# Optimization experiments

Measured on AMD Instinct MI355X. Metric: run time of the kernel, lower is better.

## Reference

```python
import jax, jax.numpy as jnp
from jax import lax
import numpy as np

N_X, N_Y, N_OBS = 30, 50, 256
ITERS, LR = 400, 0.05


def project_simplex(v):
    # Euclidean projection of a 1-D vector onto the probability simplex.
    n = v.shape[0]
    u = jnp.sort(v)[::-1]
    css = jnp.cumsum(u) - 1.0
    idx = jnp.arange(1, n + 1, dtype=v.dtype)
    rho = jnp.sum((u - css / idx) > 0)
    tau = jnp.take(css, rho - 1) / rho.astype(v.dtype)
    return jnp.maximum(v - tau, 0.0)


def worst_case(r, delta):
    # Exact value of the Ben-Tal et al. total-variation DRO inner problem:
    #   min_{eta, lam>=0} eta + delta*lam + mean_i max(-lam, r_i - eta)
    #   s.t. r_i - eta <= lam
    # = sup_{p in simplex, ||p - 1/N||_1 <= delta} p @ r
    # Closed form: move mass a = min(delta/2, (N-1)/N) from the smallest
    # entries (each holds 1/N nominal mass) onto the largest entry.
    n = r.shape[0]
    nf = jnp.asarray(n, r.dtype)
    a = jnp.minimum(delta * 0.5, (nf - 1.0) / nf)
    s = jnp.sort(r)  # ascending
    w = jnp.clip(a - jnp.arange(n, dtype=r.dtype) / nf, 0.0, 1.0 / nf)
    return jnp.mean(r) + a * jnp.max(r) - jnp.sum(w * s)


def _forward(X, Y, W, b, delta, gamma):
    Y_hat = X @ W.T + b                      # (n_obs, n_y) predictions
    ep = Y - Y_hat                           # (n_obs, n_y) residuals, shared

    def solve_one(y_hat_t):
        # Convex DRO problem per scenario, prisk = p_var: (ep_i @ z - c)^2.
        # Eliminating (eta, lam, obj_aux) analytically via worst_case(), the
        # problem reduces to min over z in simplex, c in R of
        #   worst_case((ep @ z - c)^2, delta) - gamma * (y_hat_t @ z)
        # solved with projected gradient descent (unrolled, fixed iters).
        def obj(z, c):
            r = (ep @ z - c) ** 2            # (n_obs,)
            return worst_case(r, delta) - gamma * jnp.dot(y_hat_t, z)

        z0 = jnp.full((N_Y,), 1.0 / N_Y, dtype=X.dtype)
        c0 = jnp.zeros((), dtype=X.dtype)

        def step(carry, _):
            z, c = carry
            gz, gc = jax.grad(obj, argnums=(0, 1))(z, c)
            return (project_simplex(z - LR * gz), c - LR * gc), None

        (z, _), _ = lax.scan(step, (z0, c0), None, length=ITERS)
        return z

    Z_star = jax.vmap(solve_one)(Y_hat)      # (n_obs, n_y)
    return Z_star, Y_hat


def setup_inputs() -> dict:
    key = jax.random.key(0)
    ks = jax.random.split(key, 6)
    X = jax.random.normal(ks[0], (N_OBS, N_X), dtype=jnp.float32)
    Y = jax.random.normal(ks[1], (N_OBS, N_Y), dtype=jnp.float32)
    # nn.Linear-style init scale
    W = jax.random.normal(ks[2], (N_Y, N_X), dtype=jnp.float32) / np.sqrt(N_X)
    b = jax.random.normal(ks[3], (N_Y,), dtype=jnp.float32) * 0.1
    # torch.rand(1)/5 parameters
    delta = jax.random.uniform(ks[4], (), dtype=jnp.float32) / 5.0
    gamma = jax.random.uniform(ks[5], (), dtype=jnp.float32) / 5.0
    return {"X": X, "Y": Y, "W": W, "b": b, "delta": delta, "gamma": gamma}


def reference(X, Y, W, b, delta, gamma):
    return _forward(X, Y, W, b, delta, gamma)
```

## Files before the change

### kernel.cpp

```cpp
#include <hip/hip_runtime.h>
#include <cfloat>
#include <math.h>

#define NOBS   256
#define NY     50
#define NX     30
#define NITER  400
#define LRATE  0.05f
#define CSTR   260
#define THRANK 28
#define CAND   32

typedef float f32x2 __attribute__((ext_vector_type(2)));

__device__ __forceinline__ float rl_f(float x, int k) {
  return __int_as_float(__builtin_amdgcn_readlane(__float_as_int(x), k));
}
__device__ __forceinline__ int rl_i(int x, int k) {
  return __builtin_amdgcn_readlane(x, k);
}

#define DPP_MAXSTEP(x, ctrl)                                                       \
  x = fmaxf(x, __int_as_float(__builtin_amdgcn_update_dpp(                         \
        __float_as_int(x), __float_as_int(x), (ctrl), 0xF, 0xF, false)))

#define DPP_SUMSTEP(x, ctrl, rmask)                                                \
  x += __int_as_float(__builtin_amdgcn_update_dpp(                                 \
        0, __float_as_int(x), (ctrl), (rmask), 0xF, false))

__device__ __forceinline__ float wave_sum_bcast(float x) {
  DPP_SUMSTEP(x, 0x111, 0xF);
  DPP_SUMSTEP(x, 0x112, 0xF);
  DPP_SUMSTEP(x, 0x114, 0xF);
  DPP_SUMSTEP(x, 0x118, 0xF);
  DPP_SUMSTEP(x, 0x142, 0xA);
  DPP_SUMSTEP(x, 0x143, 0xC);
  return rl_f(x, 63);
}

__global__ __launch_bounds__(512) __attribute__((amdgpu_waves_per_eu(2, 2)))
void dro_kernel(
    const float* __restrict__ X, const float* __restrict__ Y,
    const float* __restrict__ W, const float* __restrict__ Bb,
    const float* __restrict__ DLT, const float* __restrict__ GMM,
    float* __restrict__ out)
{
  __shared__ __align__(16) float smem[51 * CSTR];
  __shared__ __align__(16) unsigned rrk[NOBS];
  __shared__ __align__(16) unsigned ckey[2][128];
  __shared__ __align__(16) float wmax4[4];
  __shared__ __align__(16) int   wtie4[4];
  __shared__ int cctr[2];
  __shared__ unsigned th_key;

  float* const zs  = smem;
  float* const rdx = smem + 512;
  float* const cfs = smem + 1024;

  const int tid  = threadIdx.x;
  const int oid  = tid & 255;
  const int half = tid >> 8;
  const int lane = tid & 63;
  const int w8   = tid >> 6;
  const int wsc  = w8 & 3;
  const int t    = blockIdx.x;

  const float delta = DLT[0];
  const float gamma = GMM[0];
  const float a     = fminf(delta * 0.5f, 255.0f / 256.0f);
  const float a256  = a * 256.0f;

  f32x2 er2[25];
  {
    float xr[NX];
    #pragma unroll
    for (int k = 0; k < NX; ++k) xr[k] = X[oid * NX + k];
    #pragma unroll
    for (int j = 0; j < NY; ++j) {
      float acc = Bb[j];
      #pragma unroll
      for (int k = 0; k < NX; ++k) acc = fmaf(xr[k], W[j * NX + k], acc);
      const float e = Y[oid * NY + j] - acc;
      if (j & 1) er2[j >> 1].y = e; else er2[j >> 1].x = e;
      if (half == 0) smem[j * CSTR + oid] = e;
    }
    if (half == 0) smem[NY * CSTR + oid] = 1.0f;
  }
  float yhl;
  {
    const int jr = (lane < NY) ? lane : 0;
    float acc = Bb[jr];
    #pragma unroll
    for (int k = 0; k < NX; ++k) acc = fmaf(X[t * NX + k], W[jr * NX + k], acc);
    yhl = acc;
    if (tid < NY) out[NOBS * NY + t * NY + tid] = acc;
  }
  if (tid == 0) { th_key = 0xFFFFFFFFu; cctr[0] = 0; cctr[1] = 0; }
  if (tid < CAND) { ckey[0][tid] = 0xFFFFFFFFu; ckey[1][tid] = 0xFFFFFFFFu; }
  __syncthreads();

  f32x2 epb2[16];
  {
    const int colc = (lane < 51) ? lane : 50;
    const float* eb = &smem[colc * CSTR + wsc * 64 + half * 32];
    #pragma unroll
    for (int q = 0; q < 8; ++q) {
      const float4 e4 = *(const float4*)&eb[4 * q];
      epb2[2*q]   = (f32x2){e4.x, e4.y};
      epb2[2*q+1] = (f32x2){e4.z, e4.w};
    }
  }
  __syncthreads();

  float zv = (lane < NY) ? (1.0f / NY) : 0.0f;
  float cc = 0.0f;
  unsigned thk = 0xFFFFFFFFu;
  zs[w8 * 64 + lane] = zv;

  #pragma unroll 1
  for (int it = 0; it < NITER; ++it) {
    const int pp = it & 1;

    const float4* zp = (const float4*)&zs[w8 * 64];
    f32x2 a01 = {0.f, 0.f}, a23 = {0.f, 0.f};
    #pragma unroll
    for (int jq = 0; jq < 12; ++jq) {
      const float4 z4 = zp[jq];
      a01 = __builtin_elementwise_fma(er2[2*jq],   (f32x2){z4.x, z4.y}, a01);
      a23 = __builtin_elementwise_fma(er2[2*jq+1], (f32x2){z4.z, z4.w}, a23);
    }
    {
      const float4 z4 = zp[12];
      a01 = __builtin_elementwise_fma(er2[24], (f32x2){z4.x, z4.y}, a01);
    }
    const float u = ((a01.x + a23.x) + (a01.y + a23.y)) - cc;
    const float r = u * u;
    const unsigned key = __float_as_uint(r);

    const bool cond = (key <= thk);
    if (half == 1) {
      rrk[oid] = key;
      float m = r;
      DPP_MAXSTEP(m, 0x111); DPP_MAXSTEP(m, 0x112);
      DPP_MAXSTEP(m, 0x114); DPP_MAXSTEP(m, 0x118);
      DPP_MAXSTEP(m, 0x142); DPP_MAXSTEP(m, 0x143);
      const float mw = rl_f(m, 63);
      const int   wt = __popcll(__ballot(r == mw));
      if (lane == 0) { wmax4[wsc] = mw; wtie4[wsc] = wt; }
    } else {
      const unsigned long long cmask = __ballot(cond);
      const int cpos = __popcll(cmask & ((1ull << lane) - 1ull));
      const int cq   = __popcll(cmask);
      int base = 0;
      if (lane == 0) base = atomicAdd(&cctr[pp], cq);
      base = rl_i(base, 0);
      const int pos = base + cpos;
      if (cond && pos < 128) ckey[pp][pos] = key;
    }
    __syncthreads();

    const uint4* cp = (const uint4*)&ckey[pp][0];
    const uint4 k0_ = cp[0], k1_ = cp[1], k2_ = cp[2], k3_ = cp[3];
    const uint4 k4_ = cp[4], k5_ = cp[5], k6_ = cp[6], k7_ = cp[7];
    const int Cu = __builtin_amdgcn_readfirstlane(cctr[pp]);
    const float4 wm  = *(const float4*)wmax4;
    const int4   wtv = *(const int4*)wtie4;
    if (tid == 0) cctr[pp ^ 1] = 0;
    if (tid < CAND) ckey[pp ^ 1][tid] = 0xFFFFFFFFu;

    const float mx = fmaxf(fmaxf(wm.x, wm.y), fmaxf(wm.z, wm.w));
    const int   cm = (wm.x == mx ? wtv.x : 0) + (wm.y == mx ? wtv.y : 0)
                   + (wm.z == mx ? wtv.z : 0) + (wm.w == mx ? wtv.w : 0);
    const bool ismax = (r == mx);
    const bool valid = ((float)Cu >= a256) && (Cu <= CAND);

    int cnt;
    if (__builtin_expect(valid, 1)) {
      int n0 = 0, n1 = 0, n2 = 0, n3 = 0;
      n0 += (k0_.x < key) ? 1 : 0; n1 += (k0_.y < key) ? 1 : 0;
      n2 += (k0_.z < key) ? 1 : 0; n3 += (k0_.w < key) ? 1 : 0;
      n0 += (k1_.x < key) ? 1 : 0; n1 += (k1_.y < key) ? 1 : 0;
      n2 += (k1_.z < key) ? 1 : 0; n3 += (k1_.w < key) ? 1 : 0;
      n0 += (k2_.x < key) ? 1 : 0; n1 += (k2_.y < key) ? 1 : 0;
      n2 += (k2_.z < key) ? 1 : 0; n3 += (k2_.w < key) ? 1 : 0;
      n0 += (k3_.x < key) ? 1 : 0; n1 += (k3_.y < key) ? 1 : 0;
      n2 += (k3_.z < key) ? 1 : 0; n3 += (k3_.w < key) ? 1 : 0;
      n0 += (k4_.x < key) ? 1 : 0; n1 += (k4_.y < key) ? 1 : 0;
      n2 += (k4_.z < key) ? 1 : 0; n3 += (k4_.w < key) ? 1 : 0;
      n0 += (k5_.x < key) ? 1 : 0; n1 += (k5_.y < key) ? 1 : 0;
      n2 += (k5_.z < key) ? 1 : 0; n3 += (k5_.w < key) ? 1 : 0;
      n0 += (k6_.x < key) ? 1 : 0; n1 += (k6_.y < key) ? 1 : 0;
      n2 += (k6_.z < key) ? 1 : 0; n3 += (k6_.w < key) ? 1 : 0;
      n0 += (k7_.x < key) ? 1 : 0; n1 += (k7_.y < key) ? 1 : 0;
      n2 += (k7_.z < key) ? 1 : 0; n3 += (k7_.w < key) ? 1 : 0;
      cnt = (n0 + n1) + (n2 + n3);
    } else {
      const uint4* p = (const uint4*)rrk;
      int n0 = 0, n1 = 0, n2 = 0, n3 = 0;
      #pragma unroll 4
      for (int jq = 0; jq < 64; ++jq) {
        const uint4 k4 = p[jq];
        n0 += (k4.x < key) ? 1 : 0;
        n1 += (k4.y < key) ? 1 : 0;
        n2 += (k4.z < key) ? 1 : 0;
        n3 += (k4.w < key) ? 1 : 0;
      }
      cnt = (n0 + n1) + (n2 + n3);
    }
    if (cnt == THRANK && (!valid || cond)) th_key = key;

    const float gfac  = fminf(fmaxf((float)cnt + 1.0f - a256, 0.0f), 1.0f) * (1.0f / 256.0f);
    const float g     = gfac + (ismax ? (a / (float)cm) : 0.0f);
    const float coefv = 2.0f * u * g;

    cfs[w8 * 64 + lane] = coefv;
    const float4* cfp = (const float4*)&cfs[w8 * 64 + half * 32];
    f32x2 qa = {0.f, 0.f}, qb = {0.f, 0.f};
    #pragma unroll
    for (int q = 0; q < 8; ++q) {
      const float4 c4 = cfp[q];
      qa = __builtin_elementwise_fma((f32x2){c4.x, c4.y}, epb2[2*q],   qa);
      qb = __builtin_elementwise_fma((f32x2){c4.z, c4.w}, epb2[2*q+1], qb);
    }
    rdx[w8 * 64 + lane] = (qa.x + qb.x) + (qa.y + qb.y);
    __syncthreads();
    thk = th_key;
    const float r0 = rdx[lane],       r1 = rdx[64 + lane];
    const float r2 = rdx[128 + lane], r3 = rdx[192 + lane];
    const float r4 = rdx[256 + lane], r5 = rdx[320 + lane];
    const float r6 = rdx[384 + lane], r7 = rdx[448 + lane];
    const float s4 = ((r0 + r1) + (r2 + r3)) + ((r4 + r5) + (r6 + r7));
    cc = cc + LRATE * rl_f(s4, NY);
    const float gz = s4 - gamma * yhl;
    const float v  = zv - LRATE * gz;

    float tau = 0.0f;
    {
      bool cur = (lane < NY) && (zv > 0.0f);
      unsigned long long bal = __ballot(cur);
      int   n = __popcll(bal);
      float S = wave_sum_bcast(cur ? v : 0.0f);
      bool done = false;
      #pragma unroll 1
      for (int pass = 0; pass < 8; ++pass) {
        tau = (S - 1.0f) * __builtin_amdgcn_rcpf((float)n);
        const bool nxt = (lane < NY) && (v > tau);
        const unsigned long long nbal = __ballot(nxt);
        if (nbal == bal) { done = true; break; }
        bal = nbal;
        n   = __popcll(nbal);
        S   = wave_sum_bcast(nxt ? v : 0.0f);
      }
      if (__builtin_expect(!done, 0)) {
        bool inm = (lane < NY);
        float Sf = wave_sum_bcast(inm ? v : 0.0f);
        int   nf = NY;
        #pragma unroll 1
        for (int pass = 0; pass < 32; ++pass) {
          tau = (Sf - 1.0f) * __builtin_amdgcn_rcpf((float)nf);
          const bool nin = inm && (v > tau);
          const int  nn  = __popcll(__ballot(nin));
          if (nn == nf) break;
          Sf = wave_sum_bcast(nin ? v : 0.0f);
          nf = nn;
          inm = nin;
        }
      }
    }
    zv = (lane < NY) ? fmaxf(v - tau, 0.0f) : 0.0f;
    zs[w8 * 64 + lane] = zv;
  }

  if (w8 == 0 && lane < NY) out[t * NY + lane] = zv;

}

extern "C" void kernel_launch(void* const* d_in, const int* in_sizes, int n_in,
                              void* d_out, int out_size, void* d_ws, size_t ws_size,
                              hipStream_t stream) {
  (void)in_sizes; (void)n_in; (void)d_ws; (void)ws_size; (void)out_size;
  const float* X   = (const float*)d_in[0];
  const float* Y   = (const float*)d_in[1];
  const float* W   = (const float*)d_in[2];
  const float* B   = (const float*)d_in[3];
  const float* DLT = (const float*)d_in[4];
  const float* GMM = (const float*)d_in[5];
  float* out = (float*)d_out;
  hipLaunchKernelGGL(dro_kernel, dim3(NOBS), dim3(512), 0, stream,
                     X, Y, W, B, DLT, GMM, out);
}
```

Baseline: 763.2 us.

## Process two scenarios per block, one per 256-thread half

Each 512-thread block now solves two scenarios instead of splitting one scenario's work across both halves. Each half computes its own residual ranks, max and candidate keys, and runs the full 64-column gradient reduction. The grid drops to 128 blocks, so each thread does more per-iteration work (per-half max, candidate compaction, twice the epb registers). In exchange, the cross-half reduction traffic through shared memory goes away, and on a 256-CU part the 256 single-scenario blocks likely fit in one wave of blocks anyway.

```diff
diff --git a/kernel.cpp b/kernel.cpp
--- a/kernel.cpp
+++ b/kernel.cpp
@@ -46,12 +46,12 @@
     float* __restrict__ out)
 {
   __shared__ __align__(16) float smem[51 * CSTR];
-  __shared__ __align__(16) unsigned rrk[NOBS];
-  __shared__ __align__(16) unsigned ckey[2][128];
-  __shared__ __align__(16) float wmax4[4];
-  __shared__ __align__(16) int   wtie4[4];
-  __shared__ int cctr[2];
-  __shared__ unsigned th_key;
+  __shared__ __align__(16) unsigned rrk[2][NOBS];
+  __shared__ __align__(16) unsigned ckey[2][2][128];
+  __shared__ __align__(16) float wmax4[2][4];
+  __shared__ __align__(16) int   wtie4[2][4];
+  __shared__ int cctr[2][2];
+  __shared__ unsigned th_key[2];
 
   float* const zs  = smem;
   float* const rdx = smem + 512;
@@ -59,11 +59,11 @@
 
   const int tid  = threadIdx.x;
   const int oid  = tid & 255;
-  const int half = tid >> 8;
   const int lane = tid & 63;
   const int w8   = tid >> 6;
-  const int wsc  = w8 & 3;
-  const int t    = blockIdx.x;
+  const int sc   = w8 >> 2;
+  const int wq   = w8 & 3;
+  const int t    = blockIdx.x * 2 + sc;
 
   const float delta = DLT[0];
   const float gamma = GMM[0];
@@ -82,9 +82,9 @@
       for (int k = 0; k < NX; ++k) acc = fmaf(xr[k], W[j * NX + k], acc);
       const float e = Y[oid * NY + j] - acc;
       if (j & 1) er2[j >> 1].y = e; else er2[j >> 1].x = e;
-      if (half == 0) smem[j * CSTR + oid] = e;
-    }
-    if (half == 0) smem[NY * CSTR + oid] = 1.0f;
+      if (sc == 0) smem[j * CSTR + oid] = e;
+    }
+    if (sc == 0) smem[NY * CSTR + oid] = 1.0f;
   }
   float yhl;
   {
@@ -93,18 +93,21 @@
     #pragma unroll
     for (int k = 0; k < NX; ++k) acc = fmaf(X[t * NX + k], W[jr * NX + k], acc);
     yhl = acc;
-    if (tid < NY) out[NOBS * NY + t * NY + tid] = acc;
-  }
-  if (tid == 0) { th_key = 0xFFFFFFFFu; cctr[0] = 0; cctr[1] = 0; }
-  if (tid < CAND) { ckey[0][tid] = 0xFFFFFFFFu; ckey[1][tid] = 0xFFFFFFFFu; }
+    if (oid < NY && w8 == sc * 4) out[NOBS * NY + t * NY + oid] = acc;
+  }
+  if (tid == 0) {
+    th_key[0] = 0xFFFFFFFFu; th_key[1] = 0xFFFFFFFFu;
+    cctr[0][0] = 0; cctr[0][1] = 0; cctr[1][0] = 0; cctr[1][1] = 0;
+  }
+  if (oid < CAND) { ckey[sc][0][oid] = 0xFFFFFFFFu; ckey[sc][1][oid] = 0xFFFFFFFFu; }
   __syncthreads();
 
-  f32x2 epb2[16];
+  f32x2 epb2[32];
   {
     const int colc = (lane < 51) ? lane : 50;
-    const float* eb = &smem[colc * CSTR + wsc * 64 + half * 32];
-    #pragma unroll
-    for (int q = 0; q < 8; ++q) {
+    const float* eb = &smem[colc * CSTR + wq * 64];
+    #pragma unroll
+    for (int q = 0; q < 16; ++q) {
       const float4 e4 = *(const float4*)&eb[4 * q];
       epb2[2*q]   = (f32x2){e4.x, e4.y};
       epb2[2*q+1] = (f32x2){e4.z, e4.w};
@@ -115,13 +118,14 @@
   float zv = (lane < NY) ? (1.0f / NY) : 0.0f;
   float cc = 0.0f;
   unsigned thk = 0xFFFFFFFFu;
-  zs[w8 * 64 + lane] = zv;
+  const int wbase = sc * 256 + wq * 64;
+  zs[wbase + lane] = zv;
 
   #pragma unroll 1
   for (int it = 0; it < NITER; ++it) {
     const int pp = it & 1;
 
-    const float4* zp = (const float4*)&zs[w8 * 64];
+    const float4* zp = (const float4*)&zs[wbase];
     f32x2 a01 = {0.f, 0.f}, a23 = {0.f, 0.f};
     #pragma unroll
     for (int jq = 0; jq < 12; ++jq) {
@@ -137,36 +141,36 @@
     const float r = u * u;
     const unsigned key = __float_as_uint(r);
 
+    rrk[sc][oid] = key;
+    float m = r;
+    DPP_MAXSTEP(m, 0x111); DPP_MAXSTEP(m, 0x112);
+    DPP_MAXSTEP(m, 0x114); DPP_MAXSTEP(m, 0x118);
+    DPP_MAXSTEP(m, 0x142); DPP_MAXSTEP(m, 0x143);
+    const float mw = rl_f(m, 63);
+    const int   wt = __popcll(__ballot(r == mw));
+    if (lane == 0) { wmax4[sc][wq] = mw; wtie4[sc][wq] = wt; }
+
     const bool cond = (key <= thk);
-    if (half == 1) {
-      rrk[oid] = key;
-      float m = r;
-      DPP_MAXSTEP(m, 0x111); DPP_MAXSTEP(m, 0x112);
-      DPP_MAXSTEP(m, 0x114); DPP_MAXSTEP(m, 0x118);
-      DPP_MAXSTEP(m, 0x142); DPP_MAXSTEP(m, 0x143);
-      const float mw = rl_f(m, 63);
-      const int   wt = __popcll(__ballot(r == mw));
-      if (lane == 0) { wmax4[wsc] = mw; wtie4[wsc] = wt; }
-    } else {
+    {
       const unsigned long long cmask = __ballot(cond);
       const int cpos = __popcll(cmask & ((1ull << lane) - 1ull));
       const int cq   = __popcll(cmask);
       int base = 0;
-      if (lane == 0) base = atomicAdd(&cctr[pp], cq);
+      if (lane == 0) base = atomicAdd(&cctr[sc][pp], cq);
       base = rl_i(base, 0);
       const int pos = base + cpos;
-      if (cond && pos < 128) ckey[pp][pos] = key;
+      if (cond && pos < 128) ckey[sc][pp][pos] = key;
     }
     __syncthreads();
 
-    const uint4* cp = (const uint4*)&ckey[pp][0];
+    const uint4* cp = (const uint4*)&ckey[sc][pp][0];
     const uint4 k0_ = cp[0], k1_ = cp[1], k2_ = cp[2], k3_ = cp[3];
     const uint4 k4_ = cp[4], k5_ = cp[5], k6_ = cp[6], k7_ = cp[7];
-    const int Cu = __builtin_amdgcn_readfirstlane(cctr[pp]);
-    const float4 wm  = *(const float4*)wmax4;
-    const int4   wtv = *(const int4*)wtie4;
-    if (tid == 0) cctr[pp ^ 1] = 0;
-    if (tid < CAND) ckey[pp ^ 1][tid] = 0xFFFFFFFFu;
+    const int Cu = __builtin_amdgcn_readfirstlane(cctr[sc][pp]);
+    const float4 wm  = *(const float4*)&wmax4[sc][0];
+    const int4   wtv = *(const int4*)&wtie4[sc][0];
+    if (oid == 0) cctr[sc][pp ^ 1] = 0;
+    if (oid < CAND) ckey[sc][pp ^ 1][oid] = 0xFFFFFFFFu;
 
     const float mx = fmaxf(fmaxf(wm.x, wm.y), fmaxf(wm.z, wm.w));
     const int   cm = (wm.x == mx ? wtv.x : 0) + (wm.y == mx ? wtv.y : 0)
@@ -195,7 +199,7 @@
       n2 += (k7_.z < key) ? 1 : 0; n3 += (k7_.w < key) ? 1 : 0;
       cnt = (n0 + n1) + (n2 + n3);
     } else {
-      const uint4* p = (const uint4*)rrk;
+      const uint4* p = (const uint4*)&rrk[sc][0];
       int n0 = 0, n1 = 0, n2 = 0, n3 = 0;
       #pragma unroll 4
       for (int jq = 0; jq < 64; ++jq) {
@@ -207,29 +211,28 @@
       }
       cnt = (n0 + n1) + (n2 + n3);
     }
-    if (cnt == THRANK && (!valid || cond)) th_key = key;
+    if (cnt == THRANK && (!valid || cond)) th_key[sc] = key;
 
     const float gfac  = fminf(fmaxf((float)cnt + 1.0f - a256, 0.0f), 1.0f) * (1.0f / 256.0f);
     const float g     = gfac + (ismax ? (a / (float)cm) : 0.0f);
     const float coefv = 2.0f * u * g;
 
-    cfs[w8 * 64 + lane] = coefv;
-    const float4* cfp = (const float4*)&cfs[w8 * 64 + half * 32];
+    cfs[wbase + lane] = coefv;
+    const float4* cfp = (const float4*)&cfs[wbase];
     f32x2 qa = {0.f, 0.f}, qb = {0.f, 0.f};
     #pragma unroll
-    for (int q = 0; q < 8; ++q) {
+    for (int q = 0; q < 16; ++q) {
       const float4 c4 = cfp[q];
       qa = __builtin_elementwise_fma((f32x2){c4.x, c4.y}, epb2[2*q],   qa);
       qb = __builtin_elementwise_fma((f32x2){c4.z, c4.w}, epb2[2*q+1], qb);
     }
-    rdx[w8 * 64 + lane] = (qa.x + qb.x) + (qa.y + qb.y);
+    rdx[wbase + lane] = (qa.x + qb.x) + (qa.y + qb.y);
     __syncthreads();
-    thk = th_key;
-    const float r0 = rdx[lane],       r1 = rdx[64 + lane];
-    const float r2 = rdx[128 + lane], r3 = rdx[192 + lane];
-    const float r4 = rdx[256 + lane], r5 = rdx[320 + lane];
-    const float r6 = rdx[384 + lane], r7 = rdx[448 + lane];
-    const float s4 = ((r0 + r1) + (r2 + r3)) + ((r4 + r5) + (r6 + r7));
+    thk = th_key[sc];
+    const int rb = sc * 256;
+    const float r0 = rdx[rb + lane],       r1 = rdx[rb + 64 + lane];
+    const float r2 = rdx[rb + 128 + lane], r3 = rdx[rb + 192 + lane];
+    const float s4 = (r0 + r1) + (r2 + r3);
     cc = cc + LRATE * rl_f(s4, NY);
     const float gz = s4 - gamma * yhl;
     const float v  = zv - LRATE * gz;
@@ -268,10 +271,10 @@
       }
     }
     zv = (lane < NY) ? fmaxf(v - tau, 0.0f) : 0.0f;
-    zs[w8 * 64 + lane] = zv;
-  }
-
-  if (w8 == 0 && lane < NY) out[t * NY + lane] = zv;
+    zs[wbase + lane] = zv;
+  }
+
+  if (wq == 0 && lane < NY) out[t * NY + lane] = zv;
 
 }
 
@@ -286,6 +289,6 @@
   const float* DLT = (const float*)d_in[4];
   const float* GMM = (const float*)d_in[5];
   float* out = (float*)d_out;
-  hipLaunchKernelGGL(dro_kernel, dim3(NOBS), dim3(512), 0, stream,
+  hipLaunchKernelGGL(dro_kernel, dim3(NOBS / 2), dim3(512), 0, stream,
                      X, Y, W, B, DLT, GMM, out);
 }
```

New measurement: 810.6 us. +6.2%, slower.
